# Performance work log

Hardware: AMD Instinct MI355X
Metric: run time of the kernel (lower is better)

Reference implementation:

```python
import jax, jax.numpy as jnp
import numpy as np

DIM = 512
LEAF_DIM = 128
DEPTH = 3
NUM_LEAVES = 2 ** DEPTH  # 8
B, T = 4, 2048


def setup_inputs() -> dict:
    key = jax.random.key(0)
    ks = jax.random.split(key, 16)
    sD = DIM ** -0.5
    sF = LEAF_DIM ** -0.5
    inp = {
        "inputs": jax.random.normal(ks[0], (B, T, DIM), jnp.float32),
        "training": 1,
    }
    # per-level node (routing) params: (D, 2^d)
    for d in range(DEPTH):
        n = 2 ** d
        inp[f"wn{d}"] = jax.random.normal(ks[1 + d], (DIM, n), jnp.float32) * sD
        inp[f"bn{d}"] = jnp.zeros((n,), jnp.float32)
    # stacked leaf FFN params
    inp["w1a"] = jax.random.normal(ks[8], (NUM_LEAVES, DIM, LEAF_DIM), jnp.float32) * sD
    inp["b1a"] = jnp.zeros((NUM_LEAVES, LEAF_DIM), jnp.float32)
    inp["w1b"] = jax.random.normal(ks[9], (NUM_LEAVES, DIM, LEAF_DIM), jnp.float32) * sD
    inp["b1b"] = jnp.zeros((NUM_LEAVES, LEAF_DIM), jnp.float32)
    inp["w2"] = jax.random.normal(ks[10], (NUM_LEAVES, LEAF_DIM, DIM), jnp.float32) * sF
    inp["b2"] = jnp.zeros((NUM_LEAVES, DIM), jnp.float32)
    return inp


def reference(inputs, training, wn0, bn0, wn1, bn1, wn2, bn2, w1a, b1a, w1b, b1b, w2, b2):
    Bs, Ts, D = inputs.shape
    L = NUM_LEAVES
    sg = jax.lax.stop_gradient
    mixture = jnp.ones((Bs, Ts, L), inputs.dtype)
    for wn, bn in ((wn0, bn0), (wn1, bn1), (wn2, bn2)):
        n = wn.shape[1]  # nodes at this depth
        c = jax.nn.sigmoid(inputs @ wn + bn)  # (B,T,n)
        if training:
            # straight-through hard rounding
            c = c - sg(c) + sg(jnp.rint(c))
        else:
            c = jnp.rint(c)
        c_nc = jnp.stack([c, 1.0 - c], -1).reshape(Bs, Ts, 2 * n, 1)
        mixture = (mixture.reshape(Bs, Ts, 2 * n, L // (2 * n)) * c_nc)
    mixture = mixture.reshape(Bs, Ts, L)
    # dense per-leaf gated FFN, masked by mixture
    h = (jnp.einsum('btd,ldf->btlf', inputs, w1a) + b1a) * \
        (jnp.einsum('btd,ldf->btlf', inputs, w1b) + b1b)  # (B,T,L,F)
    y2 = jnp.einsum('btlf,lfd->btld', h, w2) + b2          # (B,T,L,D)
    y = (y2 * mixture[..., None]).sum(-2)                  # (B,T,D)
    return y
```

## Files before the change

### kernel.cpp

```cpp
#include <hip/hip_runtime.h>
#include <hip/hip_bf16.h>

#define N_TOK 8192
#define DIM   512
#define FDIM  128
#define BM    16

typedef __attribute__((ext_vector_type(8))) short short8;
typedef __attribute__((ext_vector_type(4))) float floatx4;

__device__ inline short f2bf(float f) {
    union { float f; unsigned u; } v; v.f = f;
    unsigned r = (v.u + 0x7FFF + ((v.u >> 16) & 1)) >> 16;
    return (short)r;
}

__global__ __launch_bounds__(256) void k_prep(
    const float* __restrict__ x,
    const float* __restrict__ wn0, const float* __restrict__ bn0,
    const float* __restrict__ wn1, const float* __restrict__ bn1,
    const float* __restrict__ wn2, const float* __restrict__ bn2,
    const float* __restrict__ w1a, const float* __restrict__ w1b,
    const float* __restrict__ w2,
    int* __restrict__ counts, int* __restrict__ lists,
    short* __restrict__ pw1a, short* __restrict__ pw1b, short* __restrict__ pw2)
{
    const int blk = blockIdx.x;
    if (blk < 128) {
        __shared__ int leafs[64];
        const int t = threadIdx.x;
        const int wave = t >> 6, lane = t & 63;
        const int d0 = lane * 8;
        float v0[8], v1[16], v2[32];
        #pragma unroll
        for (int j = 0; j < 8; ++j)  v0[j] = wn0[d0 + j];
        #pragma unroll
        for (int j = 0; j < 16; ++j) v1[j] = wn1[d0 * 2 + j];
        #pragma unroll
        for (int j = 0; j < 32; ++j) v2[j] = wn2[d0 * 4 + j];
        const float b0s = bn0[0];
        const float b1s[2] = {bn1[0], bn1[1]};
        const float b2s[4] = {bn2[0], bn2[1], bn2[2], bn2[3]};
        for (int i = 0; i < 16; ++i) {
            const int tok = blk * 64 + wave * 16 + i;
            const float4* xp = (const float4*)(x + tok * DIM + d0);
            const float4 xa = xp[0], xb = xp[1];
            const float xv[8] = {xa.x, xa.y, xa.z, xa.w, xb.x, xb.y, xb.z, xb.w};
            float a0 = 0.f, a1[2] = {0.f, 0.f}, a2[4] = {0.f, 0.f, 0.f, 0.f};
            #pragma unroll
            for (int j = 0; j < 8; ++j) {
                a0    += xv[j] * v0[j];
                a1[0] += xv[j] * v1[j * 2];     a1[1] += xv[j] * v1[j * 2 + 1];
                a2[0] += xv[j] * v2[j * 4];     a2[1] += xv[j] * v2[j * 4 + 1];
                a2[2] += xv[j] * v2[j * 4 + 2]; a2[3] += xv[j] * v2[j * 4 + 3];
            }
            #pragma unroll
            for (int off = 32; off >= 1; off >>= 1) {
                a0    += __shfl_xor(a0, off, 64);
                a1[0] += __shfl_xor(a1[0], off, 64);
                a1[1] += __shfl_xor(a1[1], off, 64);
                a2[0] += __shfl_xor(a2[0], off, 64);
                a2[1] += __shfl_xor(a2[1], off, 64);
                a2[2] += __shfl_xor(a2[2], off, 64);
                a2[3] += __shfl_xor(a2[3], off, 64);
            }
            int p = (a0 + b0s > 0.f) ? 0 : 1;
            const float t1 = a1[p] + b1s[p];
            p = p * 2 + ((t1 > 0.f) ? 0 : 1);
            const float t2 = a2[p] + b2s[p];
            p = p * 2 + ((t2 > 0.f) ? 0 : 1);
            if (lane == 0) leafs[wave * 16 + i] = p;
        }
        __syncthreads();
        if (t < 8) {
            const int l = t;
            int c = 0;
            for (int i = 0; i < 64; ++i) c += (leafs[i] == l);
            if (c > 0) {
                int base = atomicAdd(counts + l * 16, c);
                int j = 0;
                for (int i = 0; i < 64; ++i)
                    if (leafs[i] == l) lists[l * N_TOK + base + (j++)] = blk * 64 + i;
            }
        }
    } else {
        const int wid  = (blk - 128) * 4 + (threadIdx.x >> 6);
        const int lane = threadIdx.x & 63;
        const int q = lane >> 4, m = lane & 15;
        if (wid < 2048) {
            const float* src = (wid < 1024) ? w1a : w1b;
            short*       dst = (wid < 1024) ? pw1a : pw1b;
            const int f = wid & 1023;
            const int l = f >> 7, kb = (f >> 3) & 15, nt = f & 7;
            const float* s = src + l * 65536 + (kb * 32 + q * 8) * FDIM + nt * 16 + m;
            short8 o;
            #pragma unroll
            for (int j = 0; j < 8; ++j) o[j] = f2bf(s[j * FDIM]);
            *(short8*)(dst + f * 512 + lane * 8) = o;
        } else {
            const int f = wid - 2048;
            const int l = f >> 7, kb = (f >> 5) & 3, nt = f & 31;
            const float* s = w2 + l * 65536 + (kb * 32 + q * 8) * DIM + nt * 16 + m;
            short8 o;
            #pragma unroll
            for (int j = 0; j < 8; ++j) o[j] = f2bf(s[j * DIM]);
            *(short8*)(pw2 + f * 512 + lane * 8) = o;
        }
    }
}

__global__ __launch_bounds__(256) void k_ffn(
    const float* __restrict__ x,
    const float* __restrict__ b1a, const float* __restrict__ b1b,
    const float* __restrict__ b2,
    const short* __restrict__ pw1a, const short* __restrict__ pw1b,
    const short* __restrict__ pw2,
    const int* __restrict__ counts, const int* __restrict__ lists,
    float* __restrict__ out)
{
    const int leaf = blockIdx.y;
    const int tile = blockIdx.x;
    const int cnt  = counts[leaf * 16];
    if (tile * BM >= cnt) return;

    __shared__ int   toks[BM];
    __shared__ short xs[BM][DIM + 8];
    __shared__ short hs[BM][FDIM + 8];

    const int t = threadIdx.x;
    if (t < BM) {
        const int idx = tile * BM + t;
        toks[t] = lists[leaf * N_TOK + ((idx < cnt) ? idx : cnt - 1)];
    }
    __syncthreads();

    {
        const int row = t >> 4, c0 = (t & 15) * 32;
        const float4* src = (const float4*)(x + toks[row] * DIM + c0);
        #pragma unroll
        for (int u = 0; u < 4; ++u) {
            const float4 fa = src[u * 2], fb = src[u * 2 + 1];
            short8 o;
            o[0] = f2bf(fa.x); o[1] = f2bf(fa.y); o[2] = f2bf(fa.z); o[3] = f2bf(fa.w);
            o[4] = f2bf(fb.x); o[5] = f2bf(fb.y); o[6] = f2bf(fb.z); o[7] = f2bf(fb.w);
            *(short8*)&xs[row][c0 + u * 8] = o;
        }
    }
    __syncthreads();

    const int wave = t >> 6, lane = t & 63;
    const int qd = lane >> 4, mm = lane & 15;

    floatx4 accA0 = {0,0,0,0}, accA1 = {0,0,0,0}, accB0 = {0,0,0,0}, accB1 = {0,0,0,0};
    const int nt0 = wave * 2, nt1 = wave * 2 + 1;
    #pragma unroll
    for (int kb = 0; kb < 16; ++kb) {
        const short8 af  = *(const short8*)&xs[mm][kb * 32 + qd * 8];
        const short8 ba0 = *(const short8*)(pw1a + (((leaf * 16 + kb) * 8 + nt0) * 512) + lane * 8);
        const short8 ba1 = *(const short8*)(pw1a + (((leaf * 16 + kb) * 8 + nt1) * 512) + lane * 8);
        const short8 bb0 = *(const short8*)(pw1b + (((leaf * 16 + kb) * 8 + nt0) * 512) + lane * 8);
        const short8 bb1 = *(const short8*)(pw1b + (((leaf * 16 + kb) * 8 + nt1) * 512) + lane * 8);
        accA0 = __builtin_amdgcn_mfma_f32_16x16x32_bf16(af, ba0, accA0, 0, 0, 0);
        accA1 = __builtin_amdgcn_mfma_f32_16x16x32_bf16(af, ba1, accA1, 0, 0, 0);
        accB0 = __builtin_amdgcn_mfma_f32_16x16x32_bf16(af, bb0, accB0, 0, 0, 0);
        accB1 = __builtin_amdgcn_mfma_f32_16x16x32_bf16(af, bb1, accB1, 0, 0, 0);
    }
    {
        const int c0 = nt0 * 16 + mm, c1 = nt1 * 16 + mm;
        const float ba0 = b1a[leaf * FDIM + c0], ba1 = b1a[leaf * FDIM + c1];
        const float bb0 = b1b[leaf * FDIM + c0], bb1 = b1b[leaf * FDIM + c1];
        #pragma unroll
        for (int r = 0; r < 4; ++r) {
            const int row = qd * 4 + r;
            hs[row][c0] = f2bf((accA0[r] + ba0) * (accB0[r] + bb0));
            hs[row][c1] = f2bf((accA1[r] + ba1) * (accB1[r] + bb1));
        }
    }
    __syncthreads();

    floatx4 acc[8];
    #pragma unroll
    for (int j = 0; j < 8; ++j) acc[j] = (floatx4){0, 0, 0, 0};
    #pragma unroll
    for (int kb = 0; kb < 4; ++kb) {
        const short8 af = *(const short8*)&hs[mm][kb * 32 + qd * 8];
        #pragma unroll
        for (int j = 0; j < 8; ++j) {
            const int nt = wave * 8 + j;
            const short8 bf = *(const short8*)(pw2 + (((leaf * 4 + kb) * 32 + nt) * 512) + lane * 8);
            acc[j] = __builtin_amdgcn_mfma_f32_16x16x32_bf16(af, bf, acc[j], 0, 0, 0);
        }
    }
    const int rem = cnt - tile * BM;
    #pragma unroll
    for (int j = 0; j < 8; ++j) {
        const int col = (wave * 8 + j) * 16 + mm;
        const float bias = b2[leaf * DIM + col];
        #pragma unroll
        for (int r = 0; r < 4; ++r) {
            const int row = qd * 4 + r;
            if (row < rem) out[toks[row] * DIM + col] = acc[j][r] + bias;
        }
    }
}

extern "C" void kernel_launch(void* const* d_in, const int* in_sizes, int n_in,
                              void* d_out, int out_size, void* d_ws, size_t ws_size,
                              hipStream_t stream) {
    const float* x   = (const float*)d_in[0];
    const float* wn0 = (const float*)d_in[2];
    const float* bn0 = (const float*)d_in[3];
    const float* wn1 = (const float*)d_in[4];
    const float* bn1 = (const float*)d_in[5];
    const float* wn2 = (const float*)d_in[6];
    const float* bn2 = (const float*)d_in[7];
    const float* w1a = (const float*)d_in[8];
    const float* b1a = (const float*)d_in[9];
    const float* w1b = (const float*)d_in[10];
    const float* b1b = (const float*)d_in[11];
    const float* w2  = (const float*)d_in[12];
    const float* b2  = (const float*)d_in[13];
    float* out = (float*)d_out;

    char* ws = (char*)d_ws;
    int*   counts = (int*)(ws);
    int*   lists  = (int*)(ws + 512);
    short* pw1a   = (short*)(ws + 262656);
    short* pw1b   = (short*)(ws + 262656 + 1048576);
    short* pw2    = (short*)(ws + 262656 + 2097152);

    hipMemsetAsync(counts, 0, 512, stream);
    k_prep<<<896, 256, 0, stream>>>(x, wn0, bn0, wn1, bn1, wn2, bn2,
                                    w1a, w1b, w2, counts, lists, pw1a, pw1b, pw2);
    k_ffn<<<dim3(512, 8), 256, 0, stream>>>(x, b1a, b1b, b2, pw1a, pw1b, pw2,
                                            counts, lists, out);
}
```

Measured before the change: 137.9 us.

## Parallelize routing across token rows and double FFN token tile to 32

The routing pass now gives each token 8 threads, with 32 tokens per block spread over 256 blocks. This replaces the old scheme where each wave walked 16 tokens in sequence with full-wave shuffle reductions. The FFN kernel doubles its token tile to 32 rows and runs 8 waves per 512-thread block, split into two row halves that read the same weight fragments, so each weight fetch is better reused in cache and fewer blocks are launched. The cost is more per-thread weight loads during routing, and partially empty 32-row tiles for leaves with few tokens.

```diff
diff --git a/kernel.cpp b/kernel.cpp
--- a/kernel.cpp
+++ b/kernel.cpp
@@ -4,7 +4,7 @@
 #define N_TOK 8192
 #define DIM   512
 #define FDIM  128
-#define BM    16
+#define BM    32
 
 typedef __attribute__((ext_vector_type(8))) short short8;
 typedef __attribute__((ext_vector_type(4))) float floatx4;
@@ -26,65 +26,68 @@
     short* __restrict__ pw1a, short* __restrict__ pw1b, short* __restrict__ pw2)
 {
     const int blk = blockIdx.x;
-    if (blk < 128) {
-        __shared__ int leafs[64];
+    if (blk < 256) {
+        __shared__ int leafs[32];
         const int t = threadIdx.x;
-        const int wave = t >> 6, lane = t & 63;
-        const int d0 = lane * 8;
-        float v0[8], v1[16], v2[32];
-        #pragma unroll
-        for (int j = 0; j < 8; ++j)  v0[j] = wn0[d0 + j];
-        #pragma unroll
-        for (int j = 0; j < 16; ++j) v1[j] = wn1[d0 * 2 + j];
-        #pragma unroll
-        for (int j = 0; j < 32; ++j) v2[j] = wn2[d0 * 4 + j];
-        const float b0s = bn0[0];
-        const float b1s[2] = {bn1[0], bn1[1]};
-        const float b2s[4] = {bn2[0], bn2[1], bn2[2], bn2[3]};
-        for (int i = 0; i < 16; ++i) {
-            const int tok = blk * 64 + wave * 16 + i;
-            const float4* xp = (const float4*)(x + tok * DIM + d0);
-            const float4 xa = xp[0], xb = xp[1];
-            const float xv[8] = {xa.x, xa.y, xa.z, xa.w, xb.x, xb.y, xb.z, xb.w};
-            float a0 = 0.f, a1[2] = {0.f, 0.f}, a2[4] = {0.f, 0.f, 0.f, 0.f};
+        const int row = t >> 3, tpr = t & 7;
+        const int tok = blk * 32 + row;
+        const float* xr  = x + tok * DIM + tpr * 4;
+        const float* w0p = wn0 + tpr * 4;
+        const float* w1p = wn1 + tpr * 8;
+        const float* w2p = wn2 + tpr * 16;
+        float acc[7] = {0.f, 0.f, 0.f, 0.f, 0.f, 0.f, 0.f};
+        #pragma unroll
+        for (int u = 0; u < 16; ++u) {
+            const float4 xv = *(const float4*)(xr + u * 32);
+            const float4 w0 = *(const float4*)(w0p + u * 32);
+            const float4 wa = *(const float4*)(w1p + u * 64);
+            const float4 wb = *(const float4*)(w1p + u * 64 + 4);
+            const float4 wc = *(const float4*)(w2p + u * 128);
+            const float4 wd = *(const float4*)(w2p + u * 128 + 4);
+            const float4 we = *(const float4*)(w2p + u * 128 + 8);
+            const float4 wf = *(const float4*)(w2p + u * 128 + 12);
+            const float xs4[4] = {xv.x, xv.y, xv.z, xv.w};
+            const float w0s[4] = {w0.x, w0.y, w0.z, w0.w};
+            const float w1s[8] = {wa.x, wa.y, wa.z, wa.w, wb.x, wb.y, wb.z, wb.w};
+            const float w2s[16] = {wc.x, wc.y, wc.z, wc.w, wd.x, wd.y, wd.z, wd.w,
+                                   we.x, we.y, we.z, we.w, wf.x, wf.y, wf.z, wf.w};
             #pragma unroll
-            for (int j = 0; j < 8; ++j) {
-                a0    += xv[j] * v0[j];
-                a1[0] += xv[j] * v1[j * 2];     a1[1] += xv[j] * v1[j * 2 + 1];
-                a2[0] += xv[j] * v2[j * 4];     a2[1] += xv[j] * v2[j * 4 + 1];
-                a2[2] += xv[j] * v2[j * 4 + 2]; a2[3] += xv[j] * v2[j * 4 + 3];
+            for (int j = 0; j < 4; ++j) {
+                acc[0] += xs4[j] * w0s[j];
+                acc[1] += xs4[j] * w1s[j * 2];
+                acc[2] += xs4[j] * w1s[j * 2 + 1];
+                acc[3] += xs4[j] * w2s[j * 4];
+                acc[4] += xs4[j] * w2s[j * 4 + 1];
+                acc[5] += xs4[j] * w2s[j * 4 + 2];
+                acc[6] += xs4[j] * w2s[j * 4 + 3];
             }
-            #pragma unroll
-            for (int off = 32; off >= 1; off >>= 1) {
-                a0    += __shfl_xor(a0, off, 64);
-                a1[0] += __shfl_xor(a1[0], off, 64);
-                a1[1] += __shfl_xor(a1[1], off, 64);
-                a2[0] += __shfl_xor(a2[0], off, 64);
-                a2[1] += __shfl_xor(a2[1], off, 64);
-                a2[2] += __shfl_xor(a2[2], off, 64);
-                a2[3] += __shfl_xor(a2[3], off, 64);
-            }
-            int p = (a0 + b0s > 0.f) ? 0 : 1;
-            const float t1 = a1[p] + b1s[p];
-            p = p * 2 + ((t1 > 0.f) ? 0 : 1);
-            const float t2 = a2[p] + b2s[p];
-            p = p * 2 + ((t2 > 0.f) ? 0 : 1);
-            if (lane == 0) leafs[wave * 16 + i] = p;
-        }
+        }
+        #pragma unroll
+        for (int k = 0; k < 7; ++k) {
+            acc[k] += __shfl_xor(acc[k], 1, 64);
+            acc[k] += __shfl_xor(acc[k], 2, 64);
+            acc[k] += __shfl_xor(acc[k], 4, 64);
+        }
+        int p = (acc[0] + bn0[0] > 0.f) ? 0 : 1;
+        const float t1 = acc[1 + p] + bn1[p];
+        p = p * 2 + ((t1 > 0.f) ? 0 : 1);
+        const float t2 = acc[3 + p] + bn2[p];
+        p = p * 2 + ((t2 > 0.f) ? 0 : 1);
+        if (tpr == 0) leafs[row] = p;
         __syncthreads();
         if (t < 8) {
             const int l = t;
             int c = 0;
-            for (int i = 0; i < 64; ++i) c += (leafs[i] == l);
+            for (int i = 0; i < 32; ++i) c += (leafs[i] == l);
             if (c > 0) {
                 int base = atomicAdd(counts + l * 16, c);
                 int j = 0;
-                for (int i = 0; i < 64; ++i)
-                    if (leafs[i] == l) lists[l * N_TOK + base + (j++)] = blk * 64 + i;
+                for (int i = 0; i < 32; ++i)
+                    if (leafs[i] == l) lists[l * N_TOK + base + (j++)] = blk * 32 + i;
             }
         }
     } else {
-        const int wid  = (blk - 128) * 4 + (threadIdx.x >> 6);
+        const int wid  = (blk - 256) * 4 + (threadIdx.x >> 6);
         const int lane = threadIdx.x & 63;
         const int q = lane >> 4, m = lane & 15;
         if (wid < 2048) {
@@ -109,7 +112,7 @@
     }
 }
 
-__global__ __launch_bounds__(256) void k_ffn(
+__global__ __launch_bounds__(512) void k_ffn(
     const float* __restrict__ x,
     const float* __restrict__ b1a, const float* __restrict__ b1b,
     const float* __restrict__ b2,
@@ -149,13 +152,15 @@
     __syncthreads();
 
     const int wave = t >> 6, lane = t & 63;
+    const int mh = (wave >> 2) * 16;
+    const int wq = wave & 3;
     const int qd = lane >> 4, mm = lane & 15;
 
     floatx4 accA0 = {0,0,0,0}, accA1 = {0,0,0,0}, accB0 = {0,0,0,0}, accB1 = {0,0,0,0};
-    const int nt0 = wave * 2, nt1 = wave * 2 + 1;
+    const int nt0 = wq * 2, nt1 = wq * 2 + 1;
     #pragma unroll
     for (int kb = 0; kb < 16; ++kb) {
-        const short8 af  = *(const short8*)&xs[mm][kb * 32 + qd * 8];
+        const short8 af  = *(const short8*)&xs[mh + mm][kb * 32 + qd * 8];
         const short8 ba0 = *(const short8*)(pw1a + (((leaf * 16 + kb) * 8 + nt0) * 512) + lane * 8);
         const short8 ba1 = *(const short8*)(pw1a + (((leaf * 16 + kb) * 8 + nt1) * 512) + lane * 8);
         const short8 bb0 = *(const short8*)(pw1b + (((leaf * 16 + kb) * 8 + nt0) * 512) + lane * 8);
@@ -171,7 +176,7 @@
         const float bb0 = b1b[leaf * FDIM + c0], bb1 = b1b[leaf * FDIM + c1];
         #pragma unroll
         for (int r = 0; r < 4; ++r) {
-            const int row = qd * 4 + r;
+            const int row = mh + qd * 4 + r;
             hs[row][c0] = f2bf((accA0[r] + ba0) * (accB0[r] + bb0));
             hs[row][c1] = f2bf((accA1[r] + ba1) * (accB1[r] + bb1));
         }
@@ -183,10 +188,10 @@
     for (int j = 0; j < 8; ++j) acc[j] = (floatx4){0, 0, 0, 0};
     #pragma unroll
     for (int kb = 0; kb < 4; ++kb) {
-        const short8 af = *(const short8*)&hs[mm][kb * 32 + qd * 8];
+        const short8 af = *(const short8*)&hs[mh + mm][kb * 32 + qd * 8];
         #pragma unroll
         for (int j = 0; j < 8; ++j) {
-            const int nt = wave * 8 + j;
+            const int nt = wq * 8 + j;
             const short8 bf = *(const short8*)(pw2 + (((leaf * 4 + kb) * 32 + nt) * 512) + lane * 8);
             acc[j] = __builtin_amdgcn_mfma_f32_16x16x32_bf16(af, bf, acc[j], 0, 0, 0);
         }
@@ -194,11 +199,11 @@
     const int rem = cnt - tile * BM;
     #pragma unroll
     for (int j = 0; j < 8; ++j) {
-        const int col = (wave * 8 + j) * 16 + mm;
+        const int col = (wq * 8 + j) * 16 + mm;
         const float bias = b2[leaf * DIM + col];
         #pragma unroll
         for (int r = 0; r < 4; ++r) {
-            const int row = qd * 4 + r;
+            const int row = mh + qd * 4 + r;
             if (row < rem) out[toks[row] * DIM + col] = acc[j][r] + bias;
         }
     }
@@ -230,8 +235,8 @@
     short* pw2    = (short*)(ws + 262656 + 2097152);
 
     hipMemsetAsync(counts, 0, 512, stream);
-    k_prep<<<896, 256, 0, stream>>>(x, wn0, bn0, wn1, bn1, wn2, bn2,
-                                    w1a, w1b, w2, counts, lists, pw1a, pw1b, pw2);
-    k_ffn<<<dim3(512, 8), 256, 0, stream>>>(x, b1a, b1b, b2, pw1a, pw1b, pw2,
+    k_prep<<<1024, 256, 0, stream>>>(x, wn0, bn0, wn1, bn1, wn2, bn2,
+                                     w1a, w1b, w2, counts, lists, pw1a, pw1b, pw2);
+    k_ffn<<<dim3(256, 8), 512, 0, stream>>>(x, b1a, b1b, b2, pw1a, pw1b, pw2,
                                             counts, lists, out);
 }
```

Result: slower. 140.9 us (+2.2%).
